# Kernel optimization log

Measured on AMD Instinct MI355X. Metric: run time of the kernel, lower is better.

Reference implementation:

```python
import jax, jax.numpy as jnp
import numpy as np

D_MODEL = 1024
NUM_HEADS = 16


def setup_inputs() -> dict:
    key = jax.random.key(0)
    ks = jax.random.split(key, 5)
    B, T, d = 2, 2048, D_MODEL
    s = 1.0 / np.sqrt(d)
    return {
        "x": jax.random.normal(ks[0], (B, T, d), dtype=jnp.float32),
        "W_kqv": jax.random.normal(ks[1], (d, 3 * d), dtype=jnp.float32) * s,
        "b_kqv": jax.random.normal(ks[2], (3 * d,), dtype=jnp.float32) * 0.02,
        "W_o": jax.random.normal(ks[3], (d, d), dtype=jnp.float32) * s,
        "b_o": jax.random.normal(ks[4], (d,), dtype=jnp.float32) * 0.02,
    }


def reference(x, W_kqv, b_kqv, W_o, b_o):
    B, T, d = x.shape
    H = NUM_HEADS
    dk = d // H
    kqv = x @ W_kqv + b_kqv                      # [B, T, 3d]
    # source splits as contiguous chunks in order K, Q, V
    K, Q, V = jnp.split(kqv, 3, axis=-1)
    # [B, T, d] -> [B, H, T, dk]
    to_heads = lambda t: t.reshape(B, T, H, dk).transpose(0, 2, 1, 3)
    K, Q, V = to_heads(K), to_heads(Q), to_heads(V)
    scores = jnp.einsum("bhtd,bhsd->bhts", Q, K)  # [B, H, T, T]
    causal = jnp.triu(jnp.ones((T, T), dtype=bool), k=1)
    scores = jnp.where(causal, -jnp.inf, scores)
    attn = jax.nn.softmax(scores / jnp.sqrt(jnp.asarray(dk, x.dtype)), axis=-1)
    out = jnp.einsum("bhts,bhsd->bhtd", attn, V)  # [B, H, T, dk]
    out = out.transpose(0, 2, 1, 3).reshape(B, T, d)
    return out @ W_o + b_o
```

## Files before the change

kernel.cpp:

```cpp
#include <hip/hip_runtime.h>
#include <hip/hip_bf16.h>
#include <stdint.h>
#include <math.h>

using bf16x8 = __attribute__((ext_vector_type(8))) short;
using f32x4  = __attribute__((ext_vector_type(4))) float;
using f32x16 = __attribute__((ext_vector_type(16))) float;

#define NHEAD  16
#define DK     64
#define TSEQ   2048
#define DMODEL 1024
#define MTOT   4096

#define QSCALE 0.18033688011112042f

static __device__ __forceinline__ ushort f2bf(float f) {
  union { float f; uint32_t u; } v; v.f = f;
  return (ushort)((v.u + 0x7FFFu + ((v.u >> 16) & 1u)) >> 16);
}

static __device__ __forceinline__ uint32_t cvtpk_bf16(float lo, float hi) {
  uint32_t r;
  asm("v_cvt_pk_bf16_f32 %0, %1, %2" : "=v"(r) : "v"(lo), "v"(hi));
  return r;
}

static __device__ __forceinline__ void gload_lds16(const ushort* g, ushort* l) {
  typedef __attribute__((address_space(1))) const uint32_t gu32;
  typedef __attribute__((address_space(3))) uint32_t lu32;
  __builtin_amdgcn_global_load_lds((gu32*)g, (lu32*)l, 16, 0, 0);
}

__global__ void cvt_bf16_kernel(const float* __restrict__ in, ushort* __restrict__ out, int n) {
  int i = (blockIdx.x * 256 + threadIdx.x) * 8;
  const int stride = gridDim.x * 256 * 8;
  for (; i < n; i += stride) {
    const float4* p = (const float4*)(in + i);
    float4 a = p[0], b = p[1];
    bf16x8 v;
    v[0]=(short)f2bf(a.x); v[1]=(short)f2bf(a.y); v[2]=(short)f2bf(a.z); v[3]=(short)f2bf(a.w);
    v[4]=(short)f2bf(b.x); v[5]=(short)f2bf(b.y); v[6]=(short)f2bf(b.z); v[7]=(short)f2bf(b.w);
    *(bf16x8*)(out + i) = v;
  }
}

__global__ __launch_bounds__(256) void transpose_cvt_kernel(const float* __restrict__ W,
                                                            ushort* __restrict__ Wt, int K, int N) {
  __shared__ ushort tl[64][66];
  const int n0 = blockIdx.x * 64, k0 = blockIdx.y * 64;
  const int c = threadIdx.x & 63, r0 = threadIdx.x >> 6;
#pragma unroll
  for (int i = 0; i < 64; i += 4)
    tl[i + r0][c] = f2bf(W[(size_t)(k0 + i + r0) * N + n0 + c]);
  __syncthreads();
#pragma unroll
  for (int i = 0; i < 64; i += 4)
    Wt[(size_t)(n0 + i + r0) * K + k0 + c] = tl[c][i + r0];
}

__global__ __launch_bounds__(256) void transpose_v_kernel(const ushort* __restrict__ V,
                                                          ushort* __restrict__ Vt) {
  __shared__ ushort tl[64][66];
  const int bh = blockIdx.y, t0 = blockIdx.x * 64;
  const int c = threadIdx.x & 63, r0 = threadIdx.x >> 6;
  const ushort* Vb = V + (size_t)bh * TSEQ * DK;
  ushort* Vtb = Vt + (size_t)bh * DK * TSEQ;
#pragma unroll
  for (int i = 0; i < 64; i += 4)
    tl[i + r0][c] = Vb[(size_t)(t0 + i + r0) * DK + c];
  __syncthreads();
#pragma unroll
  for (int i = 0; i < 64; i += 4)
    Vtb[(size_t)(i + r0) * TSEQ + t0 + c] = tl[c][i + r0];
}

template <int MODE>
__global__ __launch_bounds__(256, 2)
void gemm_bt_kernel(const ushort* __restrict__ A, const ushort* __restrict__ Bt,
                    const float* __restrict__ bias,
                    ushort* __restrict__ oK, ushort* __restrict__ oQ, ushort* __restrict__ oV,
                    float* __restrict__ oF, int N, int K) {
  __shared__ ushort As[128 * 32];
  __shared__ ushort Bs[128 * 32];
  const int tid = threadIdx.x;
  const int w = tid >> 6, lane = tid & 63;
  const int m0 = blockIdx.y * 128, n0 = blockIdx.x * 128;
  const int wr = (w >> 1) * 64, wc = (w & 1) * 64;

  const int e0 = ((w * 2 + 0) * 64 + lane) * 8;
  const int e1 = ((w * 2 + 1) * 64 + lane) * 8;
  const ushort* pA0 = A  + (size_t)(m0 + (e0 >> 5)) * K + (e0 & 31);
  const ushort* pA1 = A  + (size_t)(m0 + (e1 >> 5)) * K + (e1 & 31);
  const ushort* pB0 = Bt + (size_t)(n0 + (e0 >> 5)) * K + (e0 & 31);
  const ushort* pB1 = Bt + (size_t)(n0 + (e1 >> 5)) * K + (e1 & 31);

  f32x4 acc[4][4];
#pragma unroll
  for (int i = 0; i < 4; i++)
#pragma unroll
    for (int j = 0; j < 4; j++) acc[i][j] = (f32x4){0.f, 0.f, 0.f, 0.f};

  const int aro = (wr + (lane & 15)) * 32 + (lane >> 4) * 8;
  const int bro = (wc + (lane & 15)) * 32 + (lane >> 4) * 8;

  for (int k0 = 0; k0 < K; k0 += 32) {
    __syncthreads();
    gload_lds16(pA0 + k0, &As[e0]);
    gload_lds16(pA1 + k0, &As[e1]);
    gload_lds16(pB0 + k0, &Bs[e0]);
    gload_lds16(pB1 + k0, &Bs[e1]);
    __syncthreads();
    bf16x8 af[4], bfr[4];
#pragma unroll
    for (int i = 0; i < 4; i++) af[i]  = *(const bf16x8*)&As[aro + i * 16 * 32];
#pragma unroll
    for (int j = 0; j < 4; j++) bfr[j] = *(const bf16x8*)&Bs[bro + j * 16 * 32];
#pragma unroll
    for (int i = 0; i < 4; i++)
#pragma unroll
      for (int j = 0; j < 4; j++)
        acc[i][j] = __builtin_amdgcn_mfma_f32_16x16x32_bf16(af[i], bfr[j], acc[i][j], 0, 0, 0);
  }

  const int rbase = m0 + wr + (lane >> 4) * 4;
  const int cbase = n0 + wc + (lane & 15);
#pragma unroll
  for (int i = 0; i < 4; i++) {
#pragma unroll
    for (int j = 0; j < 4; j++) {
      const int gn = cbase + j * 16;
      const float bv = bias[gn];
#pragma unroll
      for (int jj = 0; jj < 4; jj++) {
        const int gm = rbase + i * 16 + jj;
        float val = acc[i][j][jj] + bv;
        if (MODE == 0) {
          const int sel = gn >> 10, cc = gn & 1023;
          const int hh = cc >> 6, dd = cc & 63;
          const int bbx = gm >> 11, t = gm & 2047;
          if (sel == 1) val *= QSCALE;
          ushort* dst = (sel == 0) ? oK : (sel == 1) ? oQ : oV;
          dst[((size_t)((bbx * NHEAD + hh) * TSEQ + t)) * DK + dd] = f2bf(val);
        } else {
          oF[(size_t)gm * N + gn] = val;
        }
      }
    }
  }
}

__global__ __launch_bounds__(256, 2)
void attn_kernel(const ushort* __restrict__ Qb, const ushort* __restrict__ Kb,
                 const ushort* __restrict__ Vtb, ushort* __restrict__ O) {
  __shared__ ushort Ks[2][64 * 64];
  __shared__ ushort Vs[2][64 * 64];

  const int bid = blockIdx.x;
  const int xcd = bid & 7, j = bid >> 3;
  const int bh = xcd + 8 * (j >> 4);
  const int qi = 15 - (j & 15);
  const int q0 = qi * 128;
  const int bb = bh >> 4, hd = bh & 15;
  const int tid = threadIdx.x, w = tid >> 6, lane = tid & 63;
  const int l31 = lane & 31, h = lane >> 5;
  const int qrow = q0 + w * 32 + l31;

  const ushort* Qp = Qb + ((size_t)bh * TSEQ + qrow) * DK;
  bf16x8 qf[4];
#pragma unroll
  for (int c = 0; c < 4; c++)
    qf[c] = *(const bf16x8*)(Qp + c * 16 + h * 8);

  f32x16 oacc0, oacc1;
#pragma unroll
  for (int r = 0; r < 16; r++) { oacc0[r] = 0.f; oacc1[r] = 0.f; }
  float mrun = -INFINITY, lrun = 0.f;

  const int Bl0 = w * 128 + lane, Bl1 = Bl0 + 64;
  const int sr0 = Bl0 >> 3, sc0 = ((Bl0 & 7) ^ (sr0 & 7)) * 8;
  const int sr1 = Bl1 >> 3, sc1 = ((Bl1 & 7) ^ (sr1 & 7)) * 8;
  const ushort* Kp0 = Kb  + (size_t)bh * TSEQ * DK + sr0 * DK + sc0;
  const ushort* Kp1 = Kb  + (size_t)bh * TSEQ * DK + sr1 * DK + sc1;
  const ushort* Vp0 = Vtb + (size_t)bh * DK * TSEQ + sr0 * TSEQ + sc0;
  const ushort* Vp1 = Vtb + (size_t)bh * DK * TSEQ + sr1 * TSEQ + sc1;

  const int nt = 2 * qi + 2;

  gload_lds16(Kp0, &Ks[0][Bl0 * 8]);
  gload_lds16(Kp1, &Ks[0][Bl1 * 8]);
  gload_lds16(Vp0, &Vs[0][Bl0 * 8]);
  gload_lds16(Vp1, &Vs[0][Bl1 * 8]);
  asm volatile("s_waitcnt vmcnt(0)" ::: "memory");
  __builtin_amdgcn_s_barrier();

  for (int ti = 0; ti < nt; ti++) {
    const int s0 = ti * 64, cur = ti & 1;

    if (ti + 1 < nt) {
      const int sn = (ti + 1) * 64, nb = cur ^ 1;
      gload_lds16(Kp0 + sn * DK, &Ks[nb][Bl0 * 8]);
      gload_lds16(Kp1 + sn * DK, &Ks[nb][Bl1 * 8]);
      gload_lds16(Vp0 + sn, &Vs[nb][Bl0 * 8]);
      gload_lds16(Vp1 + sn, &Vs[nb][Bl1 * 8]);
    }

    const bool active = (s0 <= q0 + w * 32 + 31);
    if (active) {
      f32x16 ps0, ps1;
#pragma unroll
      for (int r = 0; r < 16; r++) { ps0[r] = 0.f; ps1[r] = 0.f; }
      const char* Kbase = (const char*)&Ks[cur][0];
      __builtin_amdgcn_s_setprio(1);
#pragma unroll
      for (int c = 0; c < 4; c++) {
        const int r0 = l31, r1 = 32 + l31;
        bf16x8 kf0 = *(const bf16x8*)(Kbase + r0 * 128 + ((c * 32 + h * 16) ^ ((r0 & 7) << 4)));
        bf16x8 kf1 = *(const bf16x8*)(Kbase + r1 * 128 + ((c * 32 + h * 16) ^ ((r1 & 7) << 4)));
        ps0 = __builtin_amdgcn_mfma_f32_32x32x16_bf16(kf0, qf[c], ps0, 0, 0, 0);
        ps1 = __builtin_amdgcn_mfma_f32_32x32x16_bf16(kf1, qf[c], ps1, 0, 0, 0);
      }
      __builtin_amdgcn_s_setprio(0);

      if (s0 + 63 > q0 + w * 32) {
#pragma unroll
        for (int r = 0; r < 16; r++) {
          const int kv0 = s0 + (r & 3) + 8 * (r >> 2) + 4 * h;
          if (kv0 > qrow)      ps0[r] = -INFINITY;
          if (kv0 + 32 > qrow) ps1[r] = -INFINITY;
        }
      }

      float pm = ps0[0];
#pragma unroll
      for (int r = 1; r < 16; r++) pm = fmaxf(pm, ps0[r]);
#pragma unroll
      for (int r = 0; r < 16; r++) pm = fmaxf(pm, ps1[r]);
      pm = fmaxf(pm, __shfl_xor(pm, 32));

      if (!__all(pm <= mrun + 8.0f)) {
        const float nm = fmaxf(mrun, pm);
        const float scl = exp2f(mrun - nm);
        lrun *= scl;
#pragma unroll
        for (int r = 0; r < 16; r++) { oacc0[r] *= scl; oacc1[r] *= scl; }
        mrun = nm;
      }

#pragma unroll
      for (int r = 0; r < 16; r++) ps0[r] = exp2f(ps0[r] - mrun);
#pragma unroll
      for (int r = 0; r < 16; r++) ps1[r] = exp2f(ps1[r] - mrun);
      float rs = 0.f;
#pragma unroll
      for (int r = 0; r < 16; r++) rs += ps0[r] + ps1[r];
      rs += __shfl_xor(rs, 32);
      lrun += rs;

      uint32_t w0[2][4], w1[2][4];
#pragma unroll
      for (int a = 0; a < 4; a++) {
        w0[0][a] = cvtpk_bf16(ps0[4 * a + 0], ps0[4 * a + 1]);
        w1[0][a] = cvtpk_bf16(ps0[4 * a + 2], ps0[4 * a + 3]);
        w0[1][a] = cvtpk_bf16(ps1[4 * a + 0], ps1[4 * a + 1]);
        w1[1][a] = cvtpk_bf16(ps1[4 * a + 2], ps1[4 * a + 3]);
      }

      const char* Vbase = (const char*)&Vs[cur][0];
#pragma unroll
      for (int s = 0; s < 2; s++) {
#pragma unroll
        for (int u = 0; u < 2; u++) {
          const int t = 2 * s + u;
          const uint32_t sw0 = h ? w0[s][2 * u] : w0[s][2 * u + 1];
          const uint32_t sw1 = h ? w1[s][2 * u] : w1[s][2 * u + 1];
          const uint32_t rx0 = (uint32_t)__shfl_xor((int)sw0, 32);
          const uint32_t rx1 = (uint32_t)__shfl_xor((int)sw1, 32);
          int4 pw;
          pw.x = h ? (int)rx0 : (int)w0[s][2 * u];
          pw.y = h ? (int)rx1 : (int)w1[s][2 * u];
          pw.z = h ? (int)w0[s][2 * u + 1] : (int)rx0;
          pw.w = h ? (int)w1[s][2 * u + 1] : (int)rx1;
          const bf16x8 pf = __builtin_bit_cast(bf16x8, pw);

          const int vr0 = l31, vr1 = 32 + l31;
          bf16x8 vf0 = *(const bf16x8*)(Vbase + vr0 * 128 + ((t * 32 + h * 16) ^ ((vr0 & 7) << 4)));
          bf16x8 vf1 = *(const bf16x8*)(Vbase + vr1 * 128 + ((t * 32 + h * 16) ^ ((vr1 & 7) << 4)));
          __builtin_amdgcn_s_setprio(1);
          oacc0 = __builtin_amdgcn_mfma_f32_32x32x16_bf16(vf0, pf, oacc0, 0, 0, 0);
          oacc1 = __builtin_amdgcn_mfma_f32_32x32x16_bf16(vf1, pf, oacc1, 0, 0, 0);
          __builtin_amdgcn_s_setprio(0);
        }
      }
    }

    asm volatile("s_waitcnt vmcnt(0)" ::: "memory");
    __builtin_amdgcn_s_barrier();
  }

  const float inv = 1.f / lrun;
  ushort* orow = O + ((size_t)bb * TSEQ + qrow) * DMODEL + hd * DK;
#pragma unroll
  for (int r = 0; r < 16; r += 2) {
    const int d0 = (r & 3) + 8 * (r >> 2) + 4 * h;
    const uint32_t v0 = (uint32_t)f2bf(oacc0[r] * inv) | ((uint32_t)f2bf(oacc0[r + 1] * inv) << 16);
    const uint32_t v1 = (uint32_t)f2bf(oacc1[r] * inv) | ((uint32_t)f2bf(oacc1[r + 1] * inv) << 16);
    *(uint32_t*)(orow + d0)      = v0;
    *(uint32_t*)(orow + 32 + d0) = v1;
  }
}

extern "C" void kernel_launch(void* const* d_in, const int* in_sizes, int n_in,
                              void* d_out, int out_size, void* d_ws, size_t ws_size,
                              hipStream_t stream) {
  (void)in_sizes; (void)n_in; (void)out_size; (void)ws_size;
  const float* x    = (const float*)d_in[0];
  const float* Wkqv = (const float*)d_in[1];
  const float* bkqv = (const float*)d_in[2];
  const float* Wo   = (const float*)d_in[3];
  const float* bo   = (const float*)d_in[4];
  float* out = (float*)d_out;

  char* ws = (char*)d_ws;
  const size_t MB = 1024 * 1024;
  ushort* x_bf   = (ushort*)(ws + 0);
  ushort* wkqv_t = (ushort*)(ws + 8 * MB);
  ushort* wo_t   = (ushort*)(ws + 14 * MB);
  ushort* Kbuf   = (ushort*)(ws + 16 * MB);
  ushort* Qbuf   = (ushort*)(ws + 24 * MB);
  ushort* Vbuf   = (ushort*)(ws + 32 * MB);
  ushort* Vtbuf  = (ushort*)(ws + 40 * MB);
  ushort* AObuf  = (ushort*)(ws + 48 * MB);

  cvt_bf16_kernel<<<2048, 256, 0, stream>>>(x, x_bf, MTOT * DMODEL);
  transpose_cvt_kernel<<<dim3(3072 / 64, 1024 / 64), 256, 0, stream>>>(Wkqv, wkqv_t, 1024, 3072);
  transpose_cvt_kernel<<<dim3(1024 / 64, 1024 / 64), 256, 0, stream>>>(Wo, wo_t, 1024, 1024);
  gemm_bt_kernel<0><<<dim3(3072 / 128, 4096 / 128), 256, 0, stream>>>(
      x_bf, wkqv_t, bkqv, Kbuf, Qbuf, Vbuf, nullptr, 3072, 1024);
  transpose_v_kernel<<<dim3(TSEQ / 64, 32), 256, 0, stream>>>(Vbuf, Vtbuf);
  attn_kernel<<<512, 256, 0, stream>>>(Qbuf, Kbuf, Vtbuf, AObuf);
  gemm_bt_kernel<1><<<dim3(1024 / 128, 4096 / 128), 256, 0, stream>>>(
      AObuf, wo_t, bo, nullptr, nullptr, nullptr, out, 1024, 1024);
}
```

Before: 217.9 us.

## Split attention KV range in two per query tile and merge partials

Each 128-row query tile's key range is split into two equal halves handled by separate blocks, doubling the grid to 1024 blocks. Each block writes unnormalized bf16 partial outputs plus running max and sum, and a new combine kernel merges them with log-sum-exp weights. Launch bounds now request 4 blocks per SM. This targets low occupancy and load imbalance across the causal triangle, at the cost of an extra kernel launch, extra global traffic for partials, and bf16 rounding of unnormalized accumulators.

```diff
diff --git a/kernel.cpp b/kernel.cpp
--- a/kernel.cpp
+++ b/kernel.cpp
@@ -18,6 +18,11 @@
 static __device__ __forceinline__ ushort f2bf(float f) {
   union { float f; uint32_t u; } v; v.f = f;
   return (ushort)((v.u + 0x7FFFu + ((v.u >> 16) & 1u)) >> 16);
+}
+
+static __device__ __forceinline__ float bf2f(ushort u) {
+  union { uint32_t u; float f; } v; v.u = ((uint32_t)u) << 16;
+  return v.f;
 }
 
 static __device__ __forceinline__ uint32_t cvtpk_bf16(float lo, float hi) {
@@ -150,21 +155,26 @@
   }
 }
 
-__global__ __launch_bounds__(256, 2)
+__global__ __launch_bounds__(256, 4)
 void attn_kernel(const ushort* __restrict__ Qb, const ushort* __restrict__ Kb,
-                 const ushort* __restrict__ Vtb, ushort* __restrict__ O) {
+                 const ushort* __restrict__ Vtb, ushort* __restrict__ Opart,
+                 float2* __restrict__ mlbuf) {
   __shared__ ushort Ks[2][64 * 64];
   __shared__ ushort Vs[2][64 * 64];
 
   const int bid = blockIdx.x;
   const int xcd = bid & 7, j = bid >> 3;
-  const int bh = xcd + 8 * (j >> 4);
-  const int qi = 15 - (j & 15);
+  const int bh = xcd + 8 * (j >> 5);
+  const int qq = j & 31;
+  const int qi = 15 - (qq >> 1);
+  const int half = qq & 1;
   const int q0 = qi * 128;
-  const int bb = bh >> 4, hd = bh & 15;
   const int tid = threadIdx.x, w = tid >> 6, lane = tid & 63;
   const int l31 = lane & 31, h = lane >> 5;
   const int qrow = q0 + w * 32 + l31;
+
+  const int t_begin = half ? (qi + 1) : 0;
+  const int ntp = qi + 1;
 
   const ushort* Qp = Qb + ((size_t)bh * TSEQ + qrow) * DK;
   bf16x8 qf[4];
@@ -185,20 +195,21 @@
   const ushort* Vp0 = Vtb + (size_t)bh * DK * TSEQ + sr0 * TSEQ + sc0;
   const ushort* Vp1 = Vtb + (size_t)bh * DK * TSEQ + sr1 * TSEQ + sc1;
 
-  const int nt = 2 * qi + 2;
-
-  gload_lds16(Kp0, &Ks[0][Bl0 * 8]);
-  gload_lds16(Kp1, &Ks[0][Bl1 * 8]);
-  gload_lds16(Vp0, &Vs[0][Bl0 * 8]);
-  gload_lds16(Vp1, &Vs[0][Bl1 * 8]);
+  {
+    const int s0 = t_begin * 64;
+    gload_lds16(Kp0 + s0 * DK, &Ks[0][Bl0 * 8]);
+    gload_lds16(Kp1 + s0 * DK, &Ks[0][Bl1 * 8]);
+    gload_lds16(Vp0 + s0, &Vs[0][Bl0 * 8]);
+    gload_lds16(Vp1 + s0, &Vs[0][Bl1 * 8]);
+  }
   asm volatile("s_waitcnt vmcnt(0)" ::: "memory");
   __builtin_amdgcn_s_barrier();
 
-  for (int ti = 0; ti < nt; ti++) {
-    const int s0 = ti * 64, cur = ti & 1;
-
-    if (ti + 1 < nt) {
-      const int sn = (ti + 1) * 64, nb = cur ^ 1;
+  for (int tt = 0; tt < ntp; tt++) {
+    const int s0 = (t_begin + tt) * 64, cur = tt & 1;
+
+    if (tt + 1 < ntp) {
+      const int sn = (t_begin + tt + 1) * 64, nb = cur ^ 1;
       gload_lds16(Kp0 + sn * DK, &Ks[nb][Bl0 * 8]);
       gload_lds16(Kp1 + sn * DK, &Ks[nb][Bl1 * 8]);
       gload_lds16(Vp0 + sn, &Vs[nb][Bl0 * 8]);
@@ -298,16 +309,35 @@
     __builtin_amdgcn_s_barrier();
   }
 
-  const float inv = 1.f / lrun;
-  ushort* orow = O + ((size_t)bb * TSEQ + qrow) * DMODEL + hd * DK;
+  const size_t rowidx = ((size_t)bh * TSEQ + qrow) * 2 + half;
+  ushort* orow = Opart + rowidx * 64;
 #pragma unroll
   for (int r = 0; r < 16; r += 2) {
     const int d0 = (r & 3) + 8 * (r >> 2) + 4 * h;
-    const uint32_t v0 = (uint32_t)f2bf(oacc0[r] * inv) | ((uint32_t)f2bf(oacc0[r + 1] * inv) << 16);
-    const uint32_t v1 = (uint32_t)f2bf(oacc1[r] * inv) | ((uint32_t)f2bf(oacc1[r + 1] * inv) << 16);
+    const uint32_t v0 = (uint32_t)f2bf(oacc0[r]) | ((uint32_t)f2bf(oacc0[r + 1]) << 16);
+    const uint32_t v1 = (uint32_t)f2bf(oacc1[r]) | ((uint32_t)f2bf(oacc1[r + 1]) << 16);
     *(uint32_t*)(orow + d0)      = v0;
     *(uint32_t*)(orow + 32 + d0) = v1;
   }
+  if (h == 0) mlbuf[rowidx] = make_float2(mrun, lrun);
+}
+
+__global__ __launch_bounds__(256) void combine_kernel(const ushort* __restrict__ Opart,
+                                                      const float2* __restrict__ mlbuf,
+                                                      ushort* __restrict__ AO) {
+  const int gid = blockIdx.x * 4 + (threadIdx.x >> 6);
+  const int lane = threadIdx.x & 63;
+  const int bh = gid >> 11, q = gid & 2047;
+  const float2 a = mlbuf[(size_t)gid * 2 + 0];
+  const float2 b = mlbuf[(size_t)gid * 2 + 1];
+  const float M = fmaxf(a.x, b.x);
+  const float wA = exp2f(a.x - M), wB = exp2f(b.x - M);
+  const float inv = 1.f / (wA * a.y + wB * b.y);
+  const float va = bf2f(Opart[(size_t)gid * 128 + lane]);
+  const float vb = bf2f(Opart[(size_t)gid * 128 + 64 + lane]);
+  const float val = (wA * va + wB * vb) * inv;
+  const int bb = bh >> 4, hd = bh & 15;
+  AO[((size_t)bb * TSEQ + q) * DMODEL + hd * DK + lane] = f2bf(val);
 }
 
 extern "C" void kernel_launch(void* const* d_in, const int* in_sizes, int n_in,
@@ -331,6 +361,8 @@
   ushort* Vbuf   = (ushort*)(ws + 32 * MB);
   ushort* Vtbuf  = (ushort*)(ws + 40 * MB);
   ushort* AObuf  = (ushort*)(ws + 48 * MB);
+  ushort* Opart  = (ushort*)(ws + 56 * MB);
+  float2* mlbuf  = (float2*)(ws + 72 * MB);
 
   cvt_bf16_kernel<<<2048, 256, 0, stream>>>(x, x_bf, MTOT * DMODEL);
   transpose_cvt_kernel<<<dim3(3072 / 64, 1024 / 64), 256, 0, stream>>>(Wkqv, wkqv_t, 1024, 3072);
@@ -338,7 +370,8 @@
   gemm_bt_kernel<0><<<dim3(3072 / 128, 4096 / 128), 256, 0, stream>>>(
       x_bf, wkqv_t, bkqv, Kbuf, Qbuf, Vbuf, nullptr, 3072, 1024);
   transpose_v_kernel<<<dim3(TSEQ / 64, 32), 256, 0, stream>>>(Vbuf, Vtbuf);
-  attn_kernel<<<512, 256, 0, stream>>>(Qbuf, Kbuf, Vtbuf, AObuf);
+  attn_kernel<<<1024, 256, 0, stream>>>(Qbuf, Kbuf, Vtbuf, Opart, mlbuf);
+  combine_kernel<<<16384, 256, 0, stream>>>(Opart, mlbuf, AObuf);
   gemm_bt_kernel<1><<<dim3(1024 / 128, 4096 / 128), 256, 0, stream>>>(
       AObuf, wo_t, bo, nullptr, nullptr, nullptr, out, 1024, 1024);
 }
```

Result: no change. 216.7 us (-0.6%).
